# Kernel optimization log

Measured on AMD Instinct MI355X. Metric: run time of the kernel, lower is better.

The kernel has to match this reference:

```python
import jax, jax.numpy as jnp
import numpy as np

B, T, C = 4, 4096, 1024
E, K, H = 8, 2, 4 * 1024


def setup_inputs() -> dict:
    key = jax.random.key(0)
    ks = jax.random.split(key, 7)
    s = lambda *sh: 1.0 / np.sqrt(sh[-2] if len(sh) > 1 else sh[-1])
    x = jax.random.normal(ks[0], (B, T, C), dtype=jnp.float32)
    router_w = jax.random.normal(ks[1], (C, E), dtype=jnp.float32) * (1.0 / np.sqrt(C))
    router_b = jnp.zeros((E,), dtype=jnp.float32)
    w1 = jax.random.normal(ks[2], (E, C, H), dtype=jnp.float32) * (1.0 / np.sqrt(C))
    b1 = jnp.zeros((E, H), dtype=jnp.float32)
    w2 = jax.random.normal(ks[3], (E, H, C), dtype=jnp.float32) * (1.0 / np.sqrt(H))
    b2 = jnp.zeros((E, C), dtype=jnp.float32)
    return {"x": x, "router_w": router_w, "router_b": router_b,
            "w1": w1, "b1": b1, "w2": w2, "b2": b2}


def reference(x, router_w, router_b, w1, b1, w2, b2):
    Bq, Tq, Cq = x.shape
    N = Bq * Tq
    logits = jnp.einsum('btc,ce->bte', x, router_w) + router_b      # [B,T,E]
    probs = jax.nn.softmax(logits, axis=-1)
    topk_vals, topk_idx = jax.lax.top_k(probs, K)                   # [B,T,K]
    x_flat = x.reshape(N, Cq)
    idx_flat = topk_idx.reshape(N, K)
    vals_flat1d = topk_vals.reshape(-1)                             # [N*K]
    # Faithful to original: weight for token t is topk_vals.view(-1)[t]
    w_tok = vals_flat1d[jnp.arange(N)]                              # [N]
    output = jnp.zeros_like(x_flat)
    for e in range(E):
        mask = (idx_flat == e).any(axis=-1)                         # [N] bool
        h = jax.nn.relu(x_flat @ w1[e] + b1[e])                     # [N,H]
        out_e = h @ w2[e] + b2[e]                                   # [N,C]
        output = output + (jnp.where(mask, w_tok, 0.0))[:, None] * out_e
    importance = probs.mean(axis=(0, 1))                            # [E]
    counts = jnp.zeros((E,), dtype=jnp.float32).at[idx_flat.reshape(-1)].add(1.0)
    load = counts / (N * K)
    aux_loss = (importance * load).sum()
    return output.reshape(Bq, Tq, Cq), aux_loss
```

## Files before the change

kernel.cpp:

```cpp
#include <hip/hip_runtime.h>
#include <hip/hip_bf16.h>

#define N_TOK 16384
#define C_DIM 1024
#define H_DIM 4096
#define E_NUM 8
#define NK_TOT 32768

typedef unsigned short u16;
typedef unsigned int u32;
typedef float f4 __attribute__((ext_vector_type(4)));
typedef __bf16 bf8 __attribute__((ext_vector_type(8)));

union V16 { f4 f; bf8 b; };

__device__ __forceinline__ u16 f2bf(float x) {
  u32 u = __builtin_bit_cast(u32, x);
  u = (u + 0x7fffu + ((u >> 16) & 1u)) >> 16;
  return (u16)u;
}

__global__ __launch_bounds__(256) void cvt_x_k(const float* __restrict__ src, u16* __restrict__ dst) {
  const size_t g = (size_t)blockIdx.x * 256 + threadIdx.x;
  const f4 v = ((const f4*)src)[g];
  u32 lo = (u32)f2bf(v[0]) | ((u32)f2bf(v[1]) << 16);
  u32 hi = (u32)f2bf(v[2]) | ((u32)f2bf(v[3]) << 16);
  ((uint2*)dst)[g] = make_uint2(lo, hi);
}

__global__ __launch_bounds__(256) void transpose_cvt_k(const float* __restrict__ src, u16* __restrict__ dst,
                                                       int R, int S) {
  __shared__ float tile[64][65];
  const size_t eoff = (size_t)blockIdx.z * R * S;
  const int s0 = blockIdx.x * 64, r0 = blockIdx.y * 64;
  for (int p = threadIdx.x; p < 4096; p += 256) {
    int r = p >> 6, s = p & 63;
    tile[r][s] = src[eoff + (size_t)(r0 + r) * S + (s0 + s)];
  }
  __syncthreads();
  for (int p = threadIdx.x; p < 4096; p += 256) {
    int sN = p >> 6, rN = p & 63;
    dst[eoff + (size_t)(s0 + sN) * R + (r0 + rN)] = f2bf(tile[rN][sN]);
  }
}

__global__ __launch_bounds__(256) void router_k(const float* __restrict__ x, const float* __restrict__ rw,
                                                const float* __restrict__ rb, int* __restrict__ idx,
                                                float* __restrict__ vals, u32* __restrict__ cnt,
                                                float* __restrict__ imp) {
  __shared__ float s_imp[E_NUM];
  __shared__ u32 s_cnt[E_NUM];
  if (threadIdx.x < E_NUM) { s_imp[threadIdx.x] = 0.f; s_cnt[threadIdx.x] = 0u; }
  __syncthreads();
  const int wave = threadIdx.x >> 6, lane = threadIdx.x & 63;
  const int t = blockIdx.x * 4 + wave;
  const float* xr = x + (size_t)t * C_DIM;
  float a[E_NUM] = {0.f, 0.f, 0.f, 0.f, 0.f, 0.f, 0.f, 0.f};
  for (int c = lane; c < C_DIM; c += 64) {
    float xv = xr[c];
    const float* w = rw + c * E_NUM;
#pragma unroll
    for (int e = 0; e < E_NUM; ++e) a[e] = fmaf(xv, w[e], a[e]);
  }
#pragma unroll
  for (int e = 0; e < E_NUM; ++e) {
#pragma unroll
    for (int off = 32; off > 0; off >>= 1) a[e] += __shfl_xor(a[e], off, 64);
  }
  if (lane == 0) {
    float p[E_NUM]; float m = -1e30f, s = 0.f;
#pragma unroll
    for (int e = 0; e < E_NUM; ++e) { p[e] = a[e] + rb[e]; m = fmaxf(m, p[e]); }
#pragma unroll
    for (int e = 0; e < E_NUM; ++e) { p[e] = expf(p[e] - m); s += p[e]; }
    const float inv = 1.f / s;
#pragma unroll
    for (int e = 0; e < E_NUM; ++e) p[e] *= inv;
    int e0 = 0; float v0 = p[0];
#pragma unroll
    for (int e = 1; e < E_NUM; ++e) if (p[e] > v0) { v0 = p[e]; e0 = e; }
    int e1 = -1; float v1 = -1e30f;
#pragma unroll
    for (int e = 0; e < E_NUM; ++e) if (e != e0 && p[e] > v1) { v1 = p[e]; e1 = e; }
    idx[2 * t] = e0; idx[2 * t + 1] = e1;
    vals[2 * t] = v0; vals[2 * t + 1] = v1;
    atomicAdd(&s_cnt[e0], 1u); atomicAdd(&s_cnt[e1], 1u);
#pragma unroll
    for (int e = 0; e < E_NUM; ++e) atomicAdd(&s_imp[e], p[e]);
  }
  __syncthreads();
  if (threadIdx.x < E_NUM) {
    atomicAdd(&cnt[threadIdx.x], s_cnt[threadIdx.x]);
    atomicAdd(&imp[threadIdx.x], s_imp[threadIdx.x]);
  }
}

__global__ void offsets_k(const u32* __restrict__ cnt, int* __restrict__ off) {
  if (threadIdx.x == 0) {
    int s = 0;
    for (int e = 0; e < E_NUM; ++e) { off[e] = s; s += (int)cnt[e]; }
    off[E_NUM] = s;
  }
}

__global__ __launch_bounds__(256) void scatter_k(const int* __restrict__ idx, u32* __restrict__ cursor,
                                                 int* __restrict__ tl) {
  __shared__ u32 lcnt[E_NUM];
  __shared__ u32 base[E_NUM];
  if (threadIdx.x < E_NUM) lcnt[threadIdx.x] = 0u;
  __syncthreads();
  const int t = blockIdx.x * 256 + threadIdx.x;
  const int e0 = idx[2 * t], e1 = idx[2 * t + 1];
  const u32 p0 = atomicAdd(&lcnt[e0], 1u);
  const u32 p1 = atomicAdd(&lcnt[e1], 1u);
  __syncthreads();
  if (threadIdx.x < E_NUM) base[threadIdx.x] = atomicAdd(&cursor[threadIdx.x], lcnt[threadIdx.x]);
  __syncthreads();
  tl[e0 * N_TOK + (int)(base[e0] + p0)] = t;
  tl[e1 * N_TOK + (int)(base[e1] + p1)] = t;
}

template <int MODE>
__global__ __launch_bounds__(256, 2) void moe_gemm(
    const u16* __restrict__ A_base, const u16* __restrict__ Bt, const float* __restrict__ bias,
    u16* __restrict__ h_out, float* out_acc, const int* __restrict__ token_list,
    const u32* __restrict__ counts, const int* __restrict__ offsets,
    int K_len, int B_stride, int B_ncap, int n_base, int k_off, int A_stride, int h_stride) {
  const int e = blockIdx.z;
  const int n_e = (int)counts[e];
  const int m0 = blockIdx.x * 128;
  if (m0 >= n_e) return;
  const int off_e = offsets[e];
  const int nb = blockIdx.y * 128;

  __shared__ u16 lA[128 * 64];
  __shared__ u16 lB[128 * 64];

  const int tid = threadIdx.x;
  const int lane = tid & 63;
  const int wave = tid >> 6;

  const int sub = lane >> 3;
  const int c16 = lane & 7;
  const int gslot = c16 ^ sub;
  const u16* a_src[4];
  const u16* b_src[4];
#pragma unroll
  for (int q = 0; q < 4; ++q) {
    const int r = q * 32 + wave * 8 + sub;
    int ar = m0 + r; if (ar > n_e - 1) ar = n_e - 1;
    size_t arow;
    if (MODE == 0) arow = (size_t)token_list[e * N_TOK + ar] * A_stride;
    else           arow = (size_t)(off_e + ar) * A_stride;
    a_src[q] = A_base + arow + gslot * 8;
    b_src[q] = Bt + ((size_t)e * B_ncap + (n_base + nb + r)) * B_stride + k_off + gslot * 8;
  }

  f4 acc[4][4];
#pragma unroll
  for (int i = 0; i < 4; ++i)
#pragma unroll
    for (int j = 0; j < 4; ++j) acc[i][j] = (f4){0.f, 0.f, 0.f, 0.f};

  const int quad = lane >> 4, l16 = lane & 15;
  const int wm = (wave >> 1) * 64;
  const int wn = (wave & 1) * 64;
  const int p7 = l16 & 7;

  const int iters = K_len >> 6;
  for (int it = 0; it < iters; ++it) {
#pragma unroll
    for (int q = 0; q < 4; ++q) {
      __builtin_amdgcn_global_load_lds(
          (const __attribute__((address_space(1))) void*)a_src[q],
          (__attribute__((address_space(3))) void*)(&lA[q * 2048 + wave * 512]),
          16, 0, 0);
      __builtin_amdgcn_global_load_lds(
          (const __attribute__((address_space(1))) void*)b_src[q],
          (__attribute__((address_space(3))) void*)(&lB[q * 2048 + wave * 512]),
          16, 0, 0);
      a_src[q] += 64; b_src[q] += 64;
    }
    __syncthreads();

#pragma unroll
    for (int kk = 0; kk < 2; ++kk) {
      const int sl = (((kk << 2) | quad) ^ p7) * 8;
      V16 af[4], bfr[4];
#pragma unroll
      for (int i = 0; i < 4; ++i) {
        af[i].f  = *(const f4*)&lA[(wm + i * 16 + l16) * 64 + sl];
        bfr[i].f = *(const f4*)&lB[(wn + i * 16 + l16) * 64 + sl];
      }
#pragma unroll
      for (int i = 0; i < 4; ++i)
#pragma unroll
        for (int j = 0; j < 4; ++j)
          acc[i][j] = __builtin_amdgcn_mfma_f32_16x16x32_bf16(af[i].b, bfr[j].b, acc[i][j], 0, 0, 0);
    }
    __syncthreads();
  }

#pragma unroll
  for (int i = 0; i < 4; ++i) {
    const int lm = wm + i * 16 + quad * 4;
#pragma unroll
    for (int j = 0; j < 4; ++j) {
      const int ncol = nb + wn + j * 16 + l16;
#pragma unroll
      for (int r = 0; r < 4; ++r) {
        const int row = m0 + lm + r;
        if (row < n_e) {
          float v = acc[i][j][r];
          if (MODE == 0) {
            v += bias[e * H_DIM + n_base + ncol];
            v = fmaxf(v, 0.f);
            h_out[(size_t)(off_e + row) * h_stride + ncol] = f2bf(v);
          } else {
            const int tok = token_list[e * N_TOK + row];
            atomicAdd(&out_acc[(size_t)tok * C_DIM + ncol], v);
          }
        }
      }
    }
  }
}

__global__ __launch_bounds__(256) void final_k(float* out, const float* __restrict__ vals,
                                               const int* __restrict__ idx, const float* __restrict__ b2,
                                               const u32* __restrict__ cnt, const float* __restrict__ imp) {
  const size_t g = (size_t)blockIdx.x * 256 + threadIdx.x;
  const int t = (int)(g >> 8);
  const int c4 = (int)(g & 255);
  const float w = vals[t];
  const int e0 = idx[2 * t], e1 = idx[2 * t + 1];
  f4 a = ((const f4*)out)[g];
  f4 u = ((const f4*)(b2 + (size_t)e0 * C_DIM))[c4];
  f4 v = ((const f4*)(b2 + (size_t)e1 * C_DIM))[c4];
  f4 r;
#pragma unroll
  for (int q = 0; q < 4; ++q) r[q] = w * (a[q] + u[q] + v[q]);
  ((f4*)out)[g] = r;
  if (g == 0) {
    float aux = 0.f;
    for (int e = 0; e < E_NUM; ++e)
      aux += (imp[e] / (float)N_TOK) * ((float)cnt[e] / (float)(N_TOK * 2));
    out[(size_t)N_TOK * C_DIM] = aux;
  }
}

extern "C" void kernel_launch(void* const* d_in, const int* in_sizes, int n_in,
                              void* d_out, int out_size, void* d_ws, size_t ws_size,
                              hipStream_t stream) {
  const float* x  = (const float*)d_in[0];
  const float* rw = (const float*)d_in[1];
  const float* rb = (const float*)d_in[2];
  const float* w1 = (const float*)d_in[3];
  const float* b1 = (const float*)d_in[4];
  const float* w2 = (const float*)d_in[5];
  const float* b2 = (const float*)d_in[6];
  float* out = (float*)d_out;

  char* ws = (char*)d_ws;
  size_t off = 0;
  auto alloc = [&](size_t bytes) -> void* {
    void* p = ws + off; off += (bytes + 255) & ~(size_t)255; return p;
  };
  u16* x_bf    = (u16*)alloc((size_t)N_TOK * C_DIM * 2);
  u16* w1t     = (u16*)alloc((size_t)E_NUM * H_DIM * C_DIM * 2);
  u16* w2t     = (u16*)alloc((size_t)E_NUM * C_DIM * H_DIM * 2);
  int* tl      = (int*)alloc((size_t)E_NUM * N_TOK * 4);
  int* idx     = (int*)alloc((size_t)N_TOK * 2 * 4);
  float* vals  = (float*)alloc((size_t)N_TOK * 2 * 4);
  u32* small   = (u32*)alloc(256);
  u32* cnt     = small;
  u32* cursor  = small + 8;
  float* imp   = (float*)(small + 16);
  int* offs    = (int*)(small + 24);

  size_t rem = (ws_size > off) ? ws_size - off : 0;
  int NC = 1;
  while (NC < 32 && (size_t)NK_TOT * (H_DIM / NC) * 2 > rem) NC <<= 1;
  const int Hc = H_DIM / NC;
  u16* h_buf = (u16*)(ws + off);

  hipMemsetAsync(out, 0, (size_t)out_size * sizeof(float), stream);
  hipMemsetAsync(small, 0, 256, stream);

  cvt_x_k<<<(N_TOK * C_DIM / 4) / 256, 256, 0, stream>>>(x, x_bf);
  transpose_cvt_k<<<dim3(H_DIM / 64, C_DIM / 64, E_NUM), 256, 0, stream>>>(w1, w1t, C_DIM, H_DIM);
  transpose_cvt_k<<<dim3(C_DIM / 64, H_DIM / 64, E_NUM), 256, 0, stream>>>(w2, w2t, H_DIM, C_DIM);
  router_k<<<N_TOK / 4, 256, 0, stream>>>(x, rw, rb, idx, vals, cnt, imp);
  offsets_k<<<1, 64, 0, stream>>>(cnt, offs);
  scatter_k<<<N_TOK / 256, 256, 0, stream>>>(idx, cursor, tl);

  for (int ci = 0; ci < NC; ++ci) {
    moe_gemm<0><<<dim3(128, Hc / 128, E_NUM), 256, 0, stream>>>(
        x_bf, w1t, b1, h_buf, nullptr, tl, cnt, offs,
         C_DIM,  C_DIM,  H_DIM,
         ci * Hc,  0,  C_DIM,  Hc);
    moe_gemm<1><<<dim3(128, C_DIM / 128, E_NUM), 256, 0, stream>>>(
        h_buf, w2t, nullptr, nullptr, out, tl, cnt, offs,
         Hc,  H_DIM,  C_DIM,
         0,  ci * Hc,  Hc,  0);
  }

  final_k<<<(N_TOK * C_DIM / 4) / 256, 256, 0, stream>>>(out, vals, idx, b2, cnt, imp);
}
```

Measured before the change: 1.306 ms.

## Enlarge MoE GEMM tiles to 256x256 with double-buffered LDS pipelining

Rewrites the expert GEMM kernel to use 256x256 output tiles with 512 threads (8 waves, 128x64 per wave) and double-buffered LDS split into two 32-wide K halves. Global-to-LDS loads for upcoming K slices are issued while MFMAs run on the current slice, with explicit vmcnt waits and barriers replacing the two __syncthreads per iteration. The aim is to raise arithmetic intensity and hide load latency. In exchange it uses more LDS (64KB) and more accumulator registers per thread, which may lower occupancy, and larger M tiles waste more work on partially filled expert tiles.

```diff
diff --git a/kernel.cpp b/kernel.cpp
--- a/kernel.cpp
+++ b/kernel.cpp
@@ -121,92 +121,118 @@
 }
 
 template <int MODE>
-__global__ __launch_bounds__(256, 2) void moe_gemm(
+__global__ __launch_bounds__(512, 2) void moe_gemm(
     const u16* __restrict__ A_base, const u16* __restrict__ Bt, const float* __restrict__ bias,
     u16* __restrict__ h_out, float* out_acc, const int* __restrict__ token_list,
     const u32* __restrict__ counts, const int* __restrict__ offsets,
     int K_len, int B_stride, int B_ncap, int n_base, int k_off, int A_stride, int h_stride) {
   const int e = blockIdx.z;
   const int n_e = (int)counts[e];
-  const int m0 = blockIdx.x * 128;
+  const int m0 = blockIdx.x * 256;
   if (m0 >= n_e) return;
   const int off_e = offsets[e];
-  const int nb = blockIdx.y * 128;
-
-  __shared__ u16 lA[128 * 64];
-  __shared__ u16 lB[128 * 64];
+  const int nb = blockIdx.y * 256;
+
+  __shared__ u16 lA[2][2][8192];
+  __shared__ u16 lB[2][2][8192];
 
   const int tid = threadIdx.x;
   const int lane = tid & 63;
   const int wave = tid >> 6;
 
-  const int sub = lane >> 3;
-  const int c16 = lane & 7;
-  const int gslot = c16 ^ sub;
-  const u16* a_src[4];
-  const u16* b_src[4];
-#pragma unroll
-  for (int q = 0; q < 4; ++q) {
-    const int r = q * 32 + wave * 8 + sub;
-    int ar = m0 + r; if (ar > n_e - 1) ar = n_e - 1;
+  const u16* a_srcp[2]; const u16* b_srcp[2];
+#pragma unroll
+  for (int q = 0; q < 2; ++q) {
+    const int p = q * 512 + tid;
+    const int lrow = p >> 2;
+    const int ss = (p & 3) ^ (lrow & 3) ^ ((lrow >> 2) & 3);
+    int ar = m0 + lrow; if (ar > n_e - 1) ar = n_e - 1;
     size_t arow;
     if (MODE == 0) arow = (size_t)token_list[e * N_TOK + ar] * A_stride;
     else           arow = (size_t)(off_e + ar) * A_stride;
-    a_src[q] = A_base + arow + gslot * 8;
-    b_src[q] = Bt + ((size_t)e * B_ncap + (n_base + nb + r)) * B_stride + k_off + gslot * 8;
-  }
-
-  f4 acc[4][4];
-#pragma unroll
-  for (int i = 0; i < 4; ++i)
-#pragma unroll
-    for (int j = 0; j < 4; ++j) acc[i][j] = (f4){0.f, 0.f, 0.f, 0.f};
-
-  const int quad = lane >> 4, l16 = lane & 15;
-  const int wm = (wave >> 1) * 64;
-  const int wn = (wave & 1) * 64;
-  const int p7 = l16 & 7;
-
-  const int iters = K_len >> 6;
-  for (int it = 0; it < iters; ++it) {
-#pragma unroll
-    for (int q = 0; q < 4; ++q) {
+    a_srcp[q] = A_base + arow + ss * 8;
+    b_srcp[q] = Bt + ((size_t)e * B_ncap + (n_base + nb + lrow)) * B_stride + k_off + ss * 8;
+  }
+
+  auto STAGE = [&](int buf, int kh, int kb) {
+#pragma unroll
+    for (int q = 0; q < 2; ++q) {
       __builtin_amdgcn_global_load_lds(
-          (const __attribute__((address_space(1))) void*)a_src[q],
-          (__attribute__((address_space(3))) void*)(&lA[q * 2048 + wave * 512]),
+          (const __attribute__((address_space(1))) void*)(a_srcp[q] + kb),
+          (__attribute__((address_space(3))) void*)(&lA[buf][kh][q * 4096 + wave * 512]),
           16, 0, 0);
       __builtin_amdgcn_global_load_lds(
-          (const __attribute__((address_space(1))) void*)b_src[q],
-          (__attribute__((address_space(3))) void*)(&lB[q * 2048 + wave * 512]),
+          (const __attribute__((address_space(1))) void*)(b_srcp[q] + kb),
+          (__attribute__((address_space(3))) void*)(&lB[buf][kh][q * 4096 + wave * 512]),
           16, 0, 0);
-      a_src[q] += 64; b_src[q] += 64;
     }
-    __syncthreads();
-
-#pragma unroll
-    for (int kk = 0; kk < 2; ++kk) {
-      const int sl = (((kk << 2) | quad) ^ p7) * 8;
-      V16 af[4], bfr[4];
-#pragma unroll
-      for (int i = 0; i < 4; ++i) {
-        af[i].f  = *(const f4*)&lA[(wm + i * 16 + l16) * 64 + sl];
-        bfr[i].f = *(const f4*)&lB[(wn + i * 16 + l16) * 64 + sl];
-      }
-#pragma unroll
-      for (int i = 0; i < 4; ++i)
-#pragma unroll
-        for (int j = 0; j < 4; ++j)
-          acc[i][j] = __builtin_amdgcn_mfma_f32_16x16x32_bf16(af[i].b, bfr[j].b, acc[i][j], 0, 0, 0);
-    }
-    __syncthreads();
-  }
-
-#pragma unroll
-  for (int i = 0; i < 4; ++i) {
-    const int lm = wm + i * 16 + quad * 4;
+  };
+
+  f4 acc[8][4];
+#pragma unroll
+  for (int i = 0; i < 8; ++i)
+#pragma unroll
+    for (int j = 0; j < 4; ++j) acc[i][j] = (f4){0.f, 0.f, 0.f, 0.f};
+
+  const int quad = lane >> 4, l16 = lane & 15;
+  const int wm2 = (wave >> 2) * 128;
+  const int wn4 = (wave & 3) * 64;
+  const int slot8 = (quad ^ ((l16 & 3) ^ ((l16 >> 2) & 3))) * 8;
+
+  auto PHASE = [&](int buf, int kk) {
+    const u16* LA = &lA[buf][kk][0];
+    const u16* LB = &lB[buf][kk][0];
+    V16 af[8], bv[4];
+#pragma unroll
+    for (int i = 0; i < 8; ++i) af[i].f = *(const f4*)&LA[(wm2 + i * 16 + l16) * 32 + slot8];
+#pragma unroll
+    for (int j = 0; j < 4; ++j) bv[j].f = *(const f4*)&LB[(wn4 + j * 16 + l16) * 32 + slot8];
+#pragma unroll
+    for (int i = 0; i < 8; ++i)
+#pragma unroll
+      for (int j = 0; j < 4; ++j)
+        acc[i][j] = __builtin_amdgcn_mfma_f32_16x16x32_bf16(af[i].b, bv[j].b, acc[i][j], 0, 0, 0);
+  };
+
+  const int T = K_len >> 6;
+
+  STAGE(0, 0, 0);
+  STAGE(0, 1, 32);
+  STAGE(1, 0, 64);
+  asm volatile("s_waitcnt vmcnt(8)\n\ts_barrier" ::: "memory");
+
+  for (int kt = 0; kt + 2 < T; ++kt) {
+    const int buf = kt & 1;
+    const int kb = kt * 64;
+    STAGE(buf ^ 1, 1, kb + 96);
+    PHASE(buf, 0);
+    asm volatile("s_waitcnt vmcnt(8) lgkmcnt(0)\n\ts_barrier" ::: "memory");
+    STAGE(buf, 0, kb + 128);
+    PHASE(buf, 1);
+    asm volatile("s_waitcnt vmcnt(8) lgkmcnt(0)\n\ts_barrier" ::: "memory");
+  }
+  {
+    const int buf = (T - 2) & 1;
+    const int kb = (T - 2) * 64;
+    STAGE(buf ^ 1, 1, kb + 96);
+    PHASE(buf, 0);
+    asm volatile("s_waitcnt vmcnt(8) lgkmcnt(0)\n\ts_barrier" ::: "memory");
+    PHASE(buf, 1);
+    asm volatile("s_waitcnt vmcnt(4) lgkmcnt(0)\n\ts_barrier" ::: "memory");
+  }
+  {
+    const int buf = (T - 1) & 1;
+    PHASE(buf, 0);
+    asm volatile("s_waitcnt vmcnt(0)" ::: "memory");
+    PHASE(buf, 1);
+  }
+
+#pragma unroll
+  for (int i = 0; i < 8; ++i) {
+    const int lm = wm2 + i * 16 + quad * 4;
 #pragma unroll
     for (int j = 0; j < 4; ++j) {
-      const int ncol = nb + wn + j * 16 + l16;
+      const int ncol = nb + wn4 + j * 16 + l16;
 #pragma unroll
       for (int r = 0; r < 4; ++r) {
         const int row = m0 + lm + r;
@@ -280,7 +306,7 @@
 
   size_t rem = (ws_size > off) ? ws_size - off : 0;
   int NC = 1;
-  while (NC < 32 && (size_t)NK_TOT * (H_DIM / NC) * 2 > rem) NC <<= 1;
+  while (NC < 16 && (size_t)NK_TOT * (H_DIM / NC) * 2 > rem) NC <<= 1;
   const int Hc = H_DIM / NC;
   u16* h_buf = (u16*)(ws + off);
 
@@ -295,11 +321,11 @@
   scatter_k<<<N_TOK / 256, 256, 0, stream>>>(idx, cursor, tl);
 
   for (int ci = 0; ci < NC; ++ci) {
-    moe_gemm<0><<<dim3(128, Hc / 128, E_NUM), 256, 0, stream>>>(
+    moe_gemm<0><<<dim3(N_TOK / 256, Hc / 256, E_NUM), 512, 0, stream>>>(
         x_bf, w1t, b1, h_buf, nullptr, tl, cnt, offs,
          C_DIM,  C_DIM,  H_DIM,
          ci * Hc,  0,  C_DIM,  Hc);
-    moe_gemm<1><<<dim3(128, C_DIM / 128, E_NUM), 256, 0, stream>>>(
+    moe_gemm<1><<<dim3(N_TOK / 256, C_DIM / 256, E_NUM), 512, 0, stream>>>(
         h_buf, w2t, nullptr, nullptr, out, tl, cnt, offs,
          Hc,  H_DIM,  C_DIM,
          0,  ci * Hc,  Hc,  0);
```

Result: slower. 2.355 ms (+80.3%).

## Widen GEMM tile to 128x256 with 512 threads and XCD-aware block remap

Applied to the files above, without the earlier changes.

The grouped MoE GEMM now uses 512-thread blocks (8 waves) computing a 128x256 output tile instead of 256 threads on 128x128, which doubles reuse of each A tile loaded into LDS. Block indices are remapped so consecutive logical tiles land on the same XCD, aiming for better L2 locality of shared weight and activation tiles. Pointer arithmetic switches to 32-bit offsets, and the H-chunk cap drops from 32 to 16. The costs are more LDS per block and fewer blocks in the grid, and the epilogue must match the new wave layout.

```diff
diff --git a/kernel.cpp b/kernel.cpp
--- a/kernel.cpp
+++ b/kernel.cpp
@@ -13,6 +13,9 @@
 typedef __bf16 bf8 __attribute__((ext_vector_type(8)));
 
 union V16 { f4 f; bf8 b; };
+
+#define AS1 __attribute__((address_space(1)))
+#define AS3 __attribute__((address_space(3)))
 
 __device__ __forceinline__ u16 f2bf(float x) {
   u32 u = __builtin_bit_cast(u32, x);
@@ -120,40 +123,60 @@
   tl[e1 * N_TOK + (int)(base[e1] + p1)] = t;
 }
 
+__device__ __forceinline__ void xcd_remap(int& bx, int& by, int& bz) {
+  const u32 nx = gridDim.x, ny = gridDim.y;
+  const u32 n = nx * ny * gridDim.z;
+  const u32 l = blockIdx.x + nx * (blockIdx.y + ny * blockIdx.z);
+  const u32 q = n >> 3, r = n & 7;
+  const u32 xcd = l & 7, i = l >> 3;
+  const u32 wg = (xcd < r ? xcd * (q + 1) : r * (q + 1) + (xcd - r) * q) + i;
+  bx = (int)(wg % nx);
+  const u32 rest = wg / nx;
+  by = (int)(rest % ny);
+  bz = (int)(rest / ny);
+}
+
 template <int MODE>
-__global__ __launch_bounds__(256, 2) void moe_gemm(
+__global__ __launch_bounds__(512, 4) void moe_gemm(
     const u16* __restrict__ A_base, const u16* __restrict__ Bt, const float* __restrict__ bias,
     u16* __restrict__ h_out, float* out_acc, const int* __restrict__ token_list,
     const u32* __restrict__ counts, const int* __restrict__ offsets,
     int K_len, int B_stride, int B_ncap, int n_base, int k_off, int A_stride, int h_stride) {
-  const int e = blockIdx.z;
+  int bx, by, bz;
+  xcd_remap(bx, by, bz);
+  const int e = bz;
   const int n_e = (int)counts[e];
-  const int m0 = blockIdx.x * 128;
+  const int m0 = bx * 128;
   if (m0 >= n_e) return;
   const int off_e = offsets[e];
-  const int nb = blockIdx.y * 128;
+  const int nb = by * 256;
 
   __shared__ u16 lA[128 * 64];
-  __shared__ u16 lB[128 * 64];
+  __shared__ u16 lB[256 * 64];
 
   const int tid = threadIdx.x;
   const int lane = tid & 63;
   const int wave = tid >> 6;
 
-  const int sub = lane >> 3;
-  const int c16 = lane & 7;
+  const int sub = (tid >> 3) & 7;
+  const int c16 = tid & 7;
   const int gslot = c16 ^ sub;
-  const u16* a_src[4];
-  const u16* b_src[4];
+  u32 a_off[2];
+  u32 b_off[4];
+#pragma unroll
+  for (int q = 0; q < 2; ++q) {
+    const int r = (q * 512 + tid) >> 3;
+    int ar = m0 + r; if (ar > n_e - 1) ar = n_e - 1;
+    u32 arow;
+    if (MODE == 0) arow = (u32)token_list[e * N_TOK + ar] * (u32)A_stride;
+    else           arow = (u32)(off_e + ar) * (u32)A_stride;
+    a_off[q] = arow + (u32)(gslot * 8);
+  }
 #pragma unroll
   for (int q = 0; q < 4; ++q) {
-    const int r = q * 32 + wave * 8 + sub;
-    int ar = m0 + r; if (ar > n_e - 1) ar = n_e - 1;
-    size_t arow;
-    if (MODE == 0) arow = (size_t)token_list[e * N_TOK + ar] * A_stride;
-    else           arow = (size_t)(off_e + ar) * A_stride;
-    a_src[q] = A_base + arow + gslot * 8;
-    b_src[q] = Bt + ((size_t)e * B_ncap + (n_base + nb + r)) * B_stride + k_off + gslot * 8;
+    const int r = (q * 512 + tid) >> 3;
+    b_off[q] = (u32)(e * B_ncap + (n_base + nb + r)) * (u32)B_stride
+               + (u32)k_off + (u32)(gslot * 8);
   }
 
   f4 acc[4][4];
@@ -163,23 +186,25 @@
     for (int j = 0; j < 4; ++j) acc[i][j] = (f4){0.f, 0.f, 0.f, 0.f};
 
   const int quad = lane >> 4, l16 = lane & 15;
-  const int wm = (wave >> 1) * 64;
-  const int wn = (wave & 1) * 64;
+  const int wm = (wave >> 2) * 64;
+  const int wn = (wave & 3) * 64;
   const int p7 = l16 & 7;
 
   const int iters = K_len >> 6;
   for (int it = 0; it < iters; ++it) {
 #pragma unroll
+    for (int q = 0; q < 2; ++q) {
+      __builtin_amdgcn_global_load_lds(
+          (const AS1 void*)(A_base + a_off[q]),
+          (AS3 void*)(&lA[q * 4096 + wave * 512]), 16, 0, 0);
+      a_off[q] += 64;
+    }
+#pragma unroll
     for (int q = 0; q < 4; ++q) {
       __builtin_amdgcn_global_load_lds(
-          (const __attribute__((address_space(1))) void*)a_src[q],
-          (__attribute__((address_space(3))) void*)(&lA[q * 2048 + wave * 512]),
-          16, 0, 0);
-      __builtin_amdgcn_global_load_lds(
-          (const __attribute__((address_space(1))) void*)b_src[q],
-          (__attribute__((address_space(3))) void*)(&lB[q * 2048 + wave * 512]),
-          16, 0, 0);
-      a_src[q] += 64; b_src[q] += 64;
+          (const AS1 void*)(Bt + b_off[q]),
+          (AS3 void*)(&lB[q * 4096 + wave * 512]), 16, 0, 0);
+      b_off[q] += 64;
     }
     __syncthreads();
 
@@ -280,7 +305,7 @@
 
   size_t rem = (ws_size > off) ? ws_size - off : 0;
   int NC = 1;
-  while (NC < 32 && (size_t)NK_TOT * (H_DIM / NC) * 2 > rem) NC <<= 1;
+  while (NC < 16 && (size_t)NK_TOT * (H_DIM / NC) * 2 > rem) NC <<= 1;
   const int Hc = H_DIM / NC;
   u16* h_buf = (u16*)(ws + off);
 
@@ -295,11 +320,11 @@
   scatter_k<<<N_TOK / 256, 256, 0, stream>>>(idx, cursor, tl);
 
   for (int ci = 0; ci < NC; ++ci) {
-    moe_gemm<0><<<dim3(128, Hc / 128, E_NUM), 256, 0, stream>>>(
+    moe_gemm<0><<<dim3(N_TOK / 128, Hc / 256, E_NUM), 512, 0, stream>>>(
         x_bf, w1t, b1, h_buf, nullptr, tl, cnt, offs,
          C_DIM,  C_DIM,  H_DIM,
          ci * Hc,  0,  C_DIM,  Hc);
-    moe_gemm<1><<<dim3(128, C_DIM / 128, E_NUM), 256, 0, stream>>>(
+    moe_gemm<1><<<dim3(N_TOK / 128, C_DIM / 256, E_NUM), 512, 0, stream>>>(
         h_buf, w2t, nullptr, nullptr, out, tl, cnt, offs,
          Hc,  H_DIM,  C_DIM,
          0,  ci * Hc,  Hc,  0);
```

After: 1.431 ms. +9.6%, slower.
